# Optimization experiments

Measured on AMD Instinct MI355X. Metric: run time of the kernel, lower is better.

## Reference

```python
import jax, jax.numpy as jnp
import numpy as np

N_NODES = 100_000
N_EDGES = 1_600_000
IN_C, HID_C, OUT_C = 128, 64, 32


def gcn_conv(x, W, b, src, dst, n_nodes):
    """PyG GCNConv with add_self_loops=True, symmetric normalization.
    out = D^{-1/2} (A + I) D^{-1/2} (x @ W) + b, with D = deg(A) + 1.
    Self-loop contribution added analytically to avoid materializing loop edges."""
    h = x @ W                                            # [N, F_out]
    deg = jnp.zeros((n_nodes,), h.dtype).at[dst].add(1.0) + 1.0
    dinv = jax.lax.rsqrt(deg)                            # deg >= 1 from self-loops
    norm = dinv[src] * dinv[dst]                         # [E]
    agg = jnp.zeros_like(h).at[dst].add(h[src] * norm[:, None])
    agg = agg + h * (dinv * dinv)[:, None]               # self-loop term
    return agg + b


def setup_inputs() -> dict:
    key = jax.random.key(0)
    ks = jax.random.split(key, 9)
    x = jax.random.normal(ks[0], (N_NODES, IN_C), dtype=jnp.float32)
    edge_index = jax.random.randint(ks[1], (2, N_EDGES), 0, N_NODES, dtype=jnp.int64)
    g = lambda k, fi, fo: jax.random.normal(k, (fi, fo), jnp.float32) * np.sqrt(2.0 / (fi + fo)).astype(np.float32)
    W1 = g(ks[2], IN_C, HID_C)
    b1 = jnp.zeros((HID_C,), jnp.float32)
    W2 = g(ks[3], HID_C, OUT_C)
    b2 = jnp.zeros((OUT_C,), jnp.float32)
    Wl = g(ks[4], IN_C + HID_C + OUT_C, OUT_C)
    bl = jnp.zeros((OUT_C,), jnp.float32)
    return {"x": x, "edge_index": edge_index, "W1": W1, "b1": b1,
            "W2": W2, "b2": b2, "Wl": Wl, "bl": bl}


def reference(x, edge_index, W1, b1, W2, b2, Wl, bl):
    src, dst = edge_index[0], edge_index[1]
    n = x.shape[0]
    h1 = jax.nn.relu(gcn_conv(x, W1, b1, src, dst, n))   # dropout is identity in eval
    h2 = gcn_conv(h1, W2, b2, src, dst, n)
    cat = jnp.concatenate([x, h1, h2], axis=1)           # [N, in+hid+out]
    return jax.nn.log_softmax(cat @ Wl + bl, axis=-1)
```

## Files before the change

### kernel.cpp

```cpp
#include <hip/hip_runtime.h>
#include <hip/hip_bf16.h>
#include <hip/hip_fp16.h>

typedef __hip_bfloat16 bf16;
typedef __attribute__((ext_vector_type(8))) short short8;
typedef __attribute__((ext_vector_type(4))) float f32x4;

#define MFMA16(a, b, c) __builtin_amdgcn_mfma_f32_16x16x32_bf16((a), (b), (c), 0, 0, 0)

static __device__ __forceinline__ float ldf(const void* p, long long i, bool f32) {
    return f32 ? ((const float*)p)[i] : __bfloat162float(((const bf16*)p)[i]);
}

static __device__ __forceinline__ short f2bs(float v) {
    union { bf16 h; short s; } u; u.h = __float2bfloat16(v); return u.s;
}

static __device__ __forceinline__ unsigned int pack_bf16x2(float a, float b) {
    return (unsigned int)(unsigned short)f2bs(a) | ((unsigned int)(unsigned short)f2bs(b) << 16);
}

__global__ __launch_bounds__(256, 4)
void sniff_kernel(const void* __restrict__ x, const void* __restrict__ w,
                  const int* __restrict__ ei, int E, int* __restrict__ flags) {
    __shared__ int cnt;
    if (threadIdx.x == 0) cnt = 0;
    __syncthreads();
    if (blockIdx.x < 2) {
        const unsigned short* u = (const unsigned short*)(blockIdx.x == 0 ? x : w);
        int bad = 0;
        for (int i = threadIdx.x; i < 4096; i += 256) {
            unsigned e = (u[i] >> 7) & 0xFF;
            if (e >= 0xA0) bad++;
        }
        atomicAdd(&cnt, bad);
        __syncthreads();
        if (threadIdx.x == 0) flags[blockIdx.x] = (cnt > 16) ? 1 : 0;
    } else {
        int nz = 0;
        for (int i = threadIdx.x; i < 1024; i += 256)
            if (ei[2 * i + 1] != 0) nz++;
        atomicAdd(&cnt, nz);
        __syncthreads();
        if (threadIdx.x == 0) flags[2] = (cnt == 0) ? 1 : 0;
    }
}

static __device__ __forceinline__ int ld_src(const int* ei, int E, int e, bool i64) {
    return i64 ? ei[2 * e] : ei[e];
}
static __device__ __forceinline__ int ld_dst(const int* ei, int E, int e, bool i64) {
    return i64 ? ei[2 * (E + e)] : ei[E + e];
}


__global__ __launch_bounds__(256, 4)
void bhist_kernel(const int* __restrict__ ei, int E, const int* __restrict__ flags,
                  int shift, int NB, int* __restrict__ bucketCount) {
    __shared__ int h[256];
    for (int i = threadIdx.x; i < 256; i += 256) h[i] = 0;
    __syncthreads();
    bool i64 = flags[2] != 0;
    int base = blockIdx.x * 4096;
    for (int i = 0; i < 16; i++) {
        int e = base + i * 256 + threadIdx.x;
        if (e < E) atomicAdd(&h[ld_dst(ei, E, e, i64) >> shift], 1);
    }
    __syncthreads();
    for (int i = threadIdx.x; i < NB; i += 256)
        if (h[i]) atomicAdd(&bucketCount[i], h[i]);
}

__global__ __launch_bounds__(256, 4)
void bscan_kernel(const int* __restrict__ bucketCount, int NB,
                  int* __restrict__ bucketBase, int* __restrict__ bcursor, int E) {
    __shared__ int bs[256];
    int v = ((int)threadIdx.x < NB) ? bucketCount[threadIdx.x] : 0;
    bs[threadIdx.x] = v;
    __syncthreads();
    for (int off = 1; off < 256; off <<= 1) {
        int t = ((int)threadIdx.x >= off) ? bs[threadIdx.x - off] : 0;
        __syncthreads();
        bs[threadIdx.x] += t;
        __syncthreads();
    }
    int excl = bs[threadIdx.x] - v;
    if ((int)threadIdx.x < NB) { bucketBase[threadIdx.x] = excl; bcursor[threadIdx.x] = excl; }
    if (threadIdx.x == 0) bucketBase[NB] = E;
}

__global__ __launch_bounds__(256, 4)
void bpart_kernel(const int* __restrict__ ei, int E, const int* __restrict__ flags,
                  int shift, int NB, int* __restrict__ bcursor, int2* __restrict__ ebuf) {
    __shared__ int h[256];
    __shared__ int gofs[256];
    for (int i = threadIdx.x; i < 256; i += 256) h[i] = 0;
    __syncthreads();
    bool i64 = flags[2] != 0;
    int base = blockIdx.x * 4096;
    for (int i = 0; i < 16; i++) {
        int e = base + i * 256 + threadIdx.x;
        if (e < E) atomicAdd(&h[ld_dst(ei, E, e, i64) >> shift], 1);
    }
    __syncthreads();
    if ((int)threadIdx.x < NB) {
        int c = h[threadIdx.x];
        gofs[threadIdx.x] = c ? atomicAdd(&bcursor[threadIdx.x], c) : 0;
    }
    __syncthreads();
    for (int i = threadIdx.x; i < 256; i += 256) h[i] = 0;
    __syncthreads();
    for (int i = 0; i < 16; i++) {
        int e = base + i * 256 + threadIdx.x;
        if (e < E) {
            int s = ld_src(ei, E, e, i64), d = ld_dst(ei, E, e, i64);
            int b = d >> shift;
            int p = atomicAdd(&h[b], 1);
            ebuf[gofs[b] + p] = make_int2(s, d);
        }
    }
}

__global__ __launch_bounds__(256, 2)
void bbuild_kernel(const int2* __restrict__ ebuf, const int* __restrict__ bucketBase,
                   int shift, int N, int E, int* __restrict__ rowptr,
                   float* __restrict__ dinv, int* __restrict__ csr_src) {
    __shared__ int cnt[1024];
    __shared__ int exc[1024];
    __shared__ int bs[256];
    int b = blockIdx.x;
    int nodeBase = b << shift;
    int width = 1 << shift;
    int nn = N - nodeBase; if (nn > width) nn = width;
    int beg = bucketBase[b], end = bucketBase[b + 1];
    for (int i = threadIdx.x; i < width; i += 256) cnt[i] = 0;
    __syncthreads();
    for (int e = beg + threadIdx.x; e < end; e += 256)
        atomicAdd(&cnt[ebuf[e].y - nodeBase], 1);
    __syncthreads();
    int per = width / 256;
    int s = 0;
    int base4 = threadIdx.x * per;
    for (int i = 0; i < per; i++) s += cnt[base4 + i];
    bs[threadIdx.x] = s;
    __syncthreads();
    for (int off = 1; off < 256; off <<= 1) {
        int t = ((int)threadIdx.x >= off) ? bs[threadIdx.x - off] : 0;
        __syncthreads();
        bs[threadIdx.x] += t;
        __syncthreads();
    }
    int run = bs[threadIdx.x] - s;
    for (int i = 0; i < per; i++) { exc[base4 + i] = run; run += cnt[base4 + i]; }
    __syncthreads();
    for (int i = threadIdx.x; i < nn; i += 256) {
        int node = nodeBase + i;
        rowptr[node] = beg + exc[i];
        dinv[node] = rsqrtf((float)cnt[i] + 1.0f);
    }
    __syncthreads();
    for (int i = threadIdx.x; i < width; i += 256) cnt[i] = 0;
    __syncthreads();
    for (int e = beg + threadIdx.x; e < end; e += 256) {
        int2 v = ebuf[e];
        int l = v.y - nodeBase;
        int p = atomicAdd(&cnt[l], 1);
        csr_src[beg + exc[l] + p] = v.x;
    }
    if (b == 0 && threadIdx.x == 0) rowptr[N] = E;
}

__global__ __launch_bounds__(256, 4)
void repack_kernel(const void* __restrict__ W1, const void* __restrict__ W2,
                   const void* __restrict__ Wl, const int* __restrict__ flags,
                   bf16* __restrict__ Bp1, bf16* __restrict__ Bp2, bf16* __restrict__ Bp3) {
    bool fw = flags[1] != 0;
    const void* W; bf16* Bp; int ntiles, nc, nfrag;
    if (blockIdx.x == 0)      { W = W1; Bp = Bp1; ntiles = 4; nc = 64; nfrag = 16; }
    else if (blockIdx.x == 1) { W = W2; Bp = Bp2; ntiles = 2; nc = 32; nfrag = 4;  }
    else                      { W = Wl; Bp = Bp3; ntiles = 2; nc = 32; nfrag = 14; }
    for (int s = threadIdx.x; s < nfrag * 64; s += 256) {
        int f = s >> 6, lane = s & 63;
        int kstep = f / ntiles, ntile = f % ntiles;
        int n = ntile * 16 + (lane & 15);
        int kbase = kstep * 32 + (lane >> 4) * 8;
#pragma unroll
        for (int j = 0; j < 8; j++)
            Bp[s * 8 + j] = __float2bfloat16(ldf(W, (long long)(kbase + j) * nc + n, fw));
    }
}

__global__ __launch_bounds__(256, 4)
void cvt_x_kernel(const void* __restrict__ x, const int* __restrict__ flags,
                  short* __restrict__ xb, long long total8) {
    long long i = (long long)blockIdx.x * 256 + threadIdx.x;
    if (i >= total8) return;
    bool fx = flags[0] != 0;
    short8 o;
    if (fx) {
        const float4* xf = (const float4*)x;
        float4 a = xf[i * 2], b = xf[i * 2 + 1];
        o[0] = f2bs(a.x); o[1] = f2bs(a.y); o[2] = f2bs(a.z); o[3] = f2bs(a.w);
        o[4] = f2bs(b.x); o[5] = f2bs(b.y); o[6] = f2bs(b.z); o[7] = f2bs(b.w);
    } else {
        o = ((const short8*)x)[i];
    }
    ((short8*)xb)[i] = o;
}

__global__ __launch_bounds__(256, 3)
void gemm1_mfma_kernel(const short* __restrict__ xb, const bf16* __restrict__ Bpack,
                       const float* __restrict__ dinv, __half* __restrict__ h1g, int N) {
    int lane = threadIdx.x & 63, wave = threadIdx.x >> 6;
    int m = lane & 15, quad = lane >> 4;
    int base = blockIdx.x * 128 + wave * 32;
    if (base >= N) return;
    const short8* bp = (const short8*)Bpack;
    short8 B[16];
#pragma unroll
    for (int i = 0; i < 16; i++) B[i] = bp[i * 64 + lane];
    if (base + 32 <= N) {
#pragma unroll
        for (int t = 0; t < 2; t++) {
            int r0 = base + t * 16;
            const short* xr = &xb[(long long)(r0 + m) * 128 + quad * 8];
            short8 A[4];
#pragma unroll
            for (int k = 0; k < 4; k++) A[k] = *(const short8*)(xr + k * 32);
            f32x4 acc[4];
#pragma unroll
            for (int nt = 0; nt < 4; nt++) acc[nt] = (f32x4){0.f, 0.f, 0.f, 0.f};
#pragma unroll
            for (int k = 0; k < 4; k++) {
#pragma unroll
                for (int nt = 0; nt < 4; nt++) acc[nt] = MFMA16(A[k], B[k * 4 + nt], acc[nt]);
            }
            float dv[4];
#pragma unroll
            for (int r = 0; r < 4; r++) dv[r] = dinv[r0 + quad * 4 + r];
            __half* o = &h1g[(long long)(r0 + quad * 4) * 64 + m];
#pragma unroll
            for (int nt = 0; nt < 4; nt++) {
#pragma unroll
                for (int r = 0; r < 4; r++) o[(long long)r * 64 + nt * 16] = __float2half(acc[nt][r] * dv[r]);
            }
        }
    } else {
#pragma unroll
        for (int t = 0; t < 2; t++) {
            int r0 = base + t * 16;
            int row = r0 + m;
            short8 A[4];
#pragma unroll
            for (int k = 0; k < 4; k++) A[k] = (short8){0,0,0,0,0,0,0,0};
            if (row < N) {
                const short* xr = &xb[(long long)row * 128 + quad * 8];
#pragma unroll
                for (int k = 0; k < 4; k++) A[k] = *(const short8*)(xr + k * 32);
            }
            f32x4 acc[4];
#pragma unroll
            for (int nt = 0; nt < 4; nt++) acc[nt] = (f32x4){0.f, 0.f, 0.f, 0.f};
#pragma unroll
            for (int k = 0; k < 4; k++) {
#pragma unroll
                for (int nt = 0; nt < 4; nt++) acc[nt] = MFMA16(A[k], B[k * 4 + nt], acc[nt]);
            }
#pragma unroll
            for (int r = 0; r < 4; r++) {
                int orow = r0 + quad * 4 + r;
                if (orow < N) {
                    float dv = dinv[orow];
                    __half* o = &h1g[(long long)orow * 64 + m];
#pragma unroll
                    for (int nt = 0; nt < 4; nt++) o[nt * 16] = __float2half(acc[nt][r] * dv);
                }
            }
        }
    }
}

__global__ __launch_bounds__(256, 8)
void gather1_kernel(const unsigned int* __restrict__ h1g, const float* __restrict__ dinv,
                    const int* __restrict__ rowptr, const int* __restrict__ csr_src,
                    const void* __restrict__ b1, const int* __restrict__ flags,
                    unsigned int* __restrict__ h1b, int N) {
    bool fw = flags[1] != 0;
    int lane = threadIdx.x & 63;
    int c = lane & 31, hf = lane >> 5;
    int wv = __builtin_amdgcn_readfirstlane(threadIdx.x >> 6);
    int node = blockIdx.x * 4 + wv;
    if (node >= N) return;
    int beg = rowptr[node], end = rowptr[node + 1];
    float dvd = dinv[node];
    const unsigned int* hL = h1g + c;
    float a0 = 0.f, a1 = 0.f;
    for (int b = beg; b < end; b += 16) {
        unsigned int v[8]; float m[8];
#pragma unroll
        for (int u = 0; u < 8; u++) {
            int i0 = b + 2 * u, i1 = i0 + 1;
            int s0 = csr_src[(i0 < end) ? i0 : beg];
            int s1 = csr_src[(i1 < end) ? i1 : beg];
            float m0 = (i0 < end) ? 1.f : 0.f;
            float m1 = (i1 < end) ? 1.f : 0.f;
            int s = hf ? s1 : s0;
            m[u] = hf ? m1 : m0;
            v[u] = hL[(long long)s * 32];
        }
#pragma unroll
        for (int u = 0; u < 8; u++) {
            float2 f = __half22float2(*(const __half2*)&v[u]);
            a0 = fmaf(f.x, m[u], a0);
            a1 = fmaf(f.y, m[u], a1);
        }
    }
    a0 += __shfl_xor(a0, 32);
    a1 += __shfl_xor(a1, 32);
    if (hf == 0) {
        unsigned int gsv = h1g[(long long)node * 32 + c];
        float2 gs = __half22float2(*(const __half2*)&gsv);
        float o0 = dvd * (a0 + gs.x) + ldf(b1, 2 * c, fw);
        float o1 = dvd * (a1 + gs.y) + ldf(b1, 2 * c + 1, fw);
        h1b[(long long)node * 32 + c] = pack_bf16x2(fmaxf(o0, 0.f), fmaxf(o1, 0.f));
    }
}

__global__ __launch_bounds__(256, 4)
void gemm2_mfma_kernel(const short* __restrict__ h1b, const bf16* __restrict__ Bpack,
                       const float* __restrict__ dinv, __half* __restrict__ h2g, int N) {
    int lane = threadIdx.x & 63, wave = threadIdx.x >> 6;
    int m = lane & 15, quad = lane >> 4;
    int r0 = blockIdx.x * 64 + wave * 16;
    if (r0 >= N) return;
    const short8* bp = (const short8*)Bpack;
    short8 B[4];
#pragma unroll
    for (int i = 0; i < 4; i++) B[i] = bp[i * 64 + lane];
    f32x4 acc0 = {0.f,0.f,0.f,0.f}, acc1 = {0.f,0.f,0.f,0.f};
    if (r0 + 16 <= N) {
        const short* xr = &h1b[(long long)(r0 + m) * 64 + quad * 8];
#pragma unroll
        for (int k = 0; k < 2; k++) {
            short8 A = *(const short8*)(xr + k * 32);
            acc0 = MFMA16(A, B[k * 2 + 0], acc0);
            acc1 = MFMA16(A, B[k * 2 + 1], acc1);
        }
        float dv[4];
#pragma unroll
        for (int r = 0; r < 4; r++) dv[r] = dinv[r0 + quad * 4 + r];
        __half* o = &h2g[(long long)(r0 + quad * 4) * 32 + m];
#pragma unroll
        for (int r = 0; r < 4; r++) {
            o[(long long)r * 32]      = __float2half(acc0[r] * dv[r]);
            o[(long long)r * 32 + 16] = __float2half(acc1[r] * dv[r]);
        }
    } else {
        int row = r0 + m;
#pragma unroll
        for (int k = 0; k < 2; k++) {
            short8 A = {0,0,0,0,0,0,0,0};
            if (row < N) A = *(const short8*)&h1b[(long long)row * 64 + k * 32 + quad * 8];
            acc0 = MFMA16(A, B[k * 2 + 0], acc0);
            acc1 = MFMA16(A, B[k * 2 + 1], acc1);
        }
#pragma unroll
        for (int r = 0; r < 4; r++) {
            int orow = r0 + quad * 4 + r;
            if (orow < N) {
                float dv = dinv[orow];
                h2g[(long long)orow * 32 + m]      = __float2half(acc0[r] * dv);
                h2g[(long long)orow * 32 + 16 + m] = __float2half(acc1[r] * dv);
            }
        }
    }
}

__global__ __launch_bounds__(256, 8)
void gather2_kernel(const unsigned int* __restrict__ h2g, const float* __restrict__ dinv,
                    const int* __restrict__ rowptr, const int* __restrict__ csr_src,
                    const void* __restrict__ b2, const int* __restrict__ flags,
                    unsigned int* __restrict__ h2b, int N) {
    bool fw = flags[1] != 0;
    int lane = threadIdx.x & 63;
    int c = lane & 15, sub = lane >> 4;
    int wv = __builtin_amdgcn_readfirstlane(threadIdx.x >> 6);
    int node = blockIdx.x * 4 + wv;
    if (node >= N) return;
    int beg = rowptr[node], end = rowptr[node + 1];
    float dvd = dinv[node];
    const unsigned int* hL = h2g + c;
    float a0 = 0.f, a1 = 0.f;
    for (int b = beg; b < end; b += 16) {
        unsigned int v[4]; float m[4];
#pragma unroll
        for (int u = 0; u < 4; u++) {
            int i0 = b + 4 * u;
            int s0 = csr_src[(i0     < end) ? i0     : beg];
            int s1 = csr_src[(i0 + 1 < end) ? i0 + 1 : beg];
            int s2 = csr_src[(i0 + 2 < end) ? i0 + 2 : beg];
            int s3 = csr_src[(i0 + 3 < end) ? i0 + 3 : beg];
            int sa = (sub & 1) ? s1 : s0;
            int sb = (sub & 1) ? s3 : s2;
            int s  = (sub & 2) ? sb : sa;
            float ma = (sub & 1) ? ((i0 + 1 < end) ? 1.f : 0.f) : ((i0 < end) ? 1.f : 0.f);
            float mb = (sub & 1) ? ((i0 + 3 < end) ? 1.f : 0.f) : ((i0 + 2 < end) ? 1.f : 0.f);
            m[u] = (sub & 2) ? mb : ma;
            v[u] = hL[(long long)s * 16];
        }
#pragma unroll
        for (int u = 0; u < 4; u++) {
            float2 f = __half22float2(*(const __half2*)&v[u]);
            a0 = fmaf(f.x, m[u], a0);
            a1 = fmaf(f.y, m[u], a1);
        }
    }
    a0 += __shfl_xor(a0, 16); a1 += __shfl_xor(a1, 16);
    a0 += __shfl_xor(a0, 32); a1 += __shfl_xor(a1, 32);
    if (sub == 0) {
        unsigned int gsv = h2g[(long long)node * 16 + c];
        float2 gs = __half22float2(*(const __half2*)&gsv);
        float o0 = dvd * (a0 + gs.x) + ldf(b2, 2 * c, fw);
        float o1 = dvd * (a1 + gs.y) + ldf(b2, 2 * c + 1, fw);
        h2b[(long long)node * 16 + c] = pack_bf16x2(o0, o1);
    }
}

__global__ __launch_bounds__(256, 2)
void final_mfma_kernel(const short* __restrict__ xb, const short* __restrict__ h1b,
                       const short* __restrict__ h2b, const bf16* __restrict__ Bpack,
                       const void* __restrict__ bl, const int* __restrict__ flags,
                       void* __restrict__ out, int N) {
    bool fw = flags[1] != 0, fx = flags[0] != 0;
    int lane = threadIdx.x & 63, wave = threadIdx.x >> 6;
    int m = lane & 15, quad = lane >> 4;
    int r0 = blockIdx.x * 64 + wave * 16;
    if (r0 >= N) return;
    const short8* bp = (const short8*)Bpack;
    short8 B[14];
#pragma unroll
    for (int i = 0; i < 14; i++) B[i] = bp[i * 64 + lane];
    f32x4 acc0 = {0.f,0.f,0.f,0.f}, acc1 = {0.f,0.f,0.f,0.f};
    bool full = (r0 + 16 <= N);
    int row = r0 + m;
    bool rowok = full || (row < N);
#pragma unroll
    for (int s = 0; s < 7; s++) {
        short8 A = {0,0,0,0,0,0,0,0};
        if (rowok) {
            const short* p;
            if (s < 4)      p = &xb [(long long)row * 128 + s * 32 + quad * 8];
            else if (s < 6) p = &h1b[(long long)row * 64 + (s - 4) * 32 + quad * 8];
            else            p = &h2b[(long long)row * 32 + quad * 8];
            A = *(const short8*)p;
        }
        acc0 = MFMA16(A, B[s * 2 + 0], acc0);
        acc1 = MFMA16(A, B[s * 2 + 1], acc1);
    }
    float bl0 = ldf(bl, m, fw), bl1 = ldf(bl, m + 16, fw);
#pragma unroll
    for (int r = 0; r < 4; r++) {
        float v0 = acc0[r] + bl0, v1 = acc1[r] + bl1;
        float mx = fmaxf(v0, v1);
#pragma unroll
        for (int o = 8; o > 0; o >>= 1) mx = fmaxf(mx, __shfl_xor(mx, o));
        float sm = __expf(v0 - mx) + __expf(v1 - mx);
#pragma unroll
        for (int o = 8; o > 0; o >>= 1) sm += __shfl_xor(sm, o);
        float lse = mx + __logf(sm);
        int orow = r0 + quad * 4 + r;
        if (orow < N) {
            if (fx) {
                ((float*)out)[(long long)orow * 32 + m]      = v0 - lse;
                ((float*)out)[(long long)orow * 32 + 16 + m] = v1 - lse;
            } else {
                ((bf16*)out)[(long long)orow * 32 + m]      = __float2bfloat16(v0 - lse);
                ((bf16*)out)[(long long)orow * 32 + 16 + m] = __float2bfloat16(v1 - lse);
            }
        }
    }
}

extern "C" void kernel_launch(void* const* d_in, const int* in_sizes, int n_in,
                              void* d_out, int out_size, void* d_ws, size_t ws_size,
                              hipStream_t stream) {
    const void* x  = d_in[0];
    const int*  ei = (const int*)d_in[1];
    const void* W1 = d_in[2];
    const void* b1 = d_in[3];
    const void* W2 = d_in[4];
    const void* b2 = d_in[5];
    const void* Wl = d_in[6];
    const void* bl = d_in[7];

    int N = in_sizes[0] / 128;
    int E = in_sizes[1] / 2;

    int shift = 9;
    while (((N + (1 << shift) - 1) >> shift) > 256 && shift < 10) shift++;
    int NB = (N + (1 << shift) - 1) >> shift;

    int* ip      = (int*)d_ws;
    int* flags   = ip;
    int* bucketCount = ip + 16;
    int* bucketBase  = bucketCount + 256;
    int* bcursor     = bucketBase + 272;
    float* dinv  = (float*)(bcursor + 256);
    int* rowptr  = (int*)(dinv + N);
    bf16* Bp1    = (bf16*)(rowptr + N + 16);
    bf16* Bp2    = (bf16*)((int*)Bp1 + 4096);
    bf16* Bp3    = (bf16*)((int*)Bp2 + 1024);
    int* csr_src = (int*)Bp3 + 3584;
    short* xb    = (short*)(csr_src + E);
    int*   Ai    = (int*)xb + (size_t)N * 64;
    int2*  ebuf  = (int2*)Ai;
    __half* h1g  = (__half*)Ai;
    __half* h2g  = (__half*)Ai;
    unsigned int* h2b = (unsigned int*)(Ai + (size_t)N * 48);
    unsigned int* h1b = (unsigned int*)(Ai + (size_t)N * 64);

    hipMemsetAsync(ip, 0, (16 + 256) * sizeof(int), stream);

    sniff_kernel<<<3, 256, 0, stream>>>(x, W1, ei, E, flags);

    int nchunk = (E + 4095) / 4096;
    bhist_kernel<<<nchunk, 256, 0, stream>>>(ei, E, flags, shift, NB, bucketCount);
    bscan_kernel<<<1, 256, 0, stream>>>(bucketCount, NB, bucketBase, bcursor, E);
    bpart_kernel<<<nchunk, 256, 0, stream>>>(ei, E, flags, shift, NB, bcursor, ebuf);
    bbuild_kernel<<<NB, 256, 0, stream>>>(ebuf, bucketBase, shift, N, E, rowptr, dinv, csr_src);

    repack_kernel<<<3, 256, 0, stream>>>(W1, W2, Wl, flags, Bp1, Bp2, Bp3);

    long long total8 = (long long)N * 16;
    cvt_x_kernel<<<(int)((total8 + 255) / 256), 256, 0, stream>>>(x, flags, xb, total8);

    gemm1_mfma_kernel<<<(N + 127) / 128, 256, 0, stream>>>(xb, Bp1, dinv, h1g, N);
    gather1_kernel<<<(N + 3) / 4, 256, 0, stream>>>((const unsigned int*)h1g, dinv, rowptr, csr_src,
                                                    b1, flags, h1b, N);
    gemm2_mfma_kernel<<<(N + 63) / 64, 256, 0, stream>>>((const short*)h1b, Bp2, dinv, h2g, N);
    gather2_kernel<<<(N + 3) / 4, 256, 0, stream>>>((const unsigned int*)h2g, dinv, rowptr, csr_src,
                                                    b2, flags, h2b, N);
    final_mfma_kernel<<<(N + 63) / 64, 256, 0, stream>>>(xb, (const short*)h1b, (const short*)h2b,
                                                         Bp3, bl, flags, d_out, N);
}
```

Before: 324.8 us.

## Process two nodes per wave in gather kernels and cache edges in LDS during partition

Each wave in the two gather kernels now handles two destination nodes and interleaves their neighbor loads, so more independent gathers are in flight per wave and fewer blocks are launched. The edge-partition kernel stages the (src,dst) pairs in shared memory on the first pass instead of reading edge_index from global memory a second time. The cost is higher register pressure in the gathers, loop trip count set by the larger of the two degrees, and 32KB of LDS per partition block, which may limit occupancy.

New measurement: 330.1 us. Within noise of the previous version (+1.6%).

```diff
diff --git a/kernel.cpp b/kernel.cpp
--- a/kernel.cpp
+++ b/kernel.cpp
@@ -94,13 +94,18 @@
                   int shift, int NB, int* __restrict__ bcursor, int2* __restrict__ ebuf) {
     __shared__ int h[256];
     __shared__ int gofs[256];
+    __shared__ int2 se[4096];
     for (int i = threadIdx.x; i < 256; i += 256) h[i] = 0;
     __syncthreads();
     bool i64 = flags[2] != 0;
     int base = blockIdx.x * 4096;
     for (int i = 0; i < 16; i++) {
         int e = base + i * 256 + threadIdx.x;
-        if (e < E) atomicAdd(&h[ld_dst(ei, E, e, i64) >> shift], 1);
+        if (e < E) {
+            int s = ld_src(ei, E, e, i64), d = ld_dst(ei, E, e, i64);
+            se[i * 256 + threadIdx.x] = make_int2(s, d);
+            atomicAdd(&h[d >> shift], 1);
+        }
     }
     __syncthreads();
     if ((int)threadIdx.x < NB) {
@@ -113,10 +118,10 @@
     for (int i = 0; i < 16; i++) {
         int e = base + i * 256 + threadIdx.x;
         if (e < E) {
-            int s = ld_src(ei, E, e, i64), d = ld_dst(ei, E, e, i64);
-            int b = d >> shift;
+            int2 v = se[i * 256 + threadIdx.x];
+            int b = v.y >> shift;
             int p = atomicAdd(&h[b], 1);
-            ebuf[gofs[b] + p] = make_int2(s, d);
+            ebuf[gofs[b] + p] = v;
         }
     }
 }
@@ -283,45 +288,59 @@
 __global__ __launch_bounds__(256, 8)
 void gather1_kernel(const unsigned int* __restrict__ h1g, const float* __restrict__ dinv,
                     const int* __restrict__ rowptr, const int* __restrict__ csr_src,
-                    const void* __restrict__ b1, const int* __restrict__ flags,
+                    const void* __restrict__ bptr, const int* __restrict__ flags,
                     unsigned int* __restrict__ h1b, int N) {
     bool fw = flags[1] != 0;
     int lane = threadIdx.x & 63;
     int c = lane & 31, hf = lane >> 5;
     int wv = __builtin_amdgcn_readfirstlane(threadIdx.x >> 6);
-    int node = blockIdx.x * 4 + wv;
-    if (node >= N) return;
-    int beg = rowptr[node], end = rowptr[node + 1];
-    float dvd = dinv[node];
+    int n0 = blockIdx.x * 8 + wv * 2;
+    if (n0 >= N) return;
+    int n1 = (n0 + 1 < N) ? n0 + 1 : n0;
+    int beg0 = rowptr[n0], end0 = rowptr[n0 + 1];
+    int beg1 = rowptr[n1], end1 = rowptr[n1 + 1];
     const unsigned int* hL = h1g + c;
-    float a0 = 0.f, a1 = 0.f;
-    for (int b = beg; b < end; b += 16) {
-        unsigned int v[8]; float m[8];
+    float a00 = 0.f, a01 = 0.f, a10 = 0.f, a11 = 0.f;
+    int p0 = beg0, p1 = beg1;
+    while (p0 < end0 || p1 < end1) {
+        unsigned int v0[8], v1[8]; float m0[8], m1[8];
 #pragma unroll
         for (int u = 0; u < 8; u++) {
-            int i0 = b + 2 * u, i1 = i0 + 1;
-            int s0 = csr_src[(i0 < end) ? i0 : beg];
-            int s1 = csr_src[(i1 < end) ? i1 : beg];
-            float m0 = (i0 < end) ? 1.f : 0.f;
-            float m1 = (i1 < end) ? 1.f : 0.f;
-            int s = hf ? s1 : s0;
-            m[u] = hf ? m1 : m0;
-            v[u] = hL[(long long)s * 32];
+            int i00 = p0 + 2 * u, i01 = i00 + 1;
+            int s00 = csr_src[(i00 < end0) ? i00 : beg0];
+            int s01 = csr_src[(i01 < end0) ? i01 : beg0];
+            int sA = hf ? s01 : s00;
+            m0[u] = hf ? ((i01 < end0) ? 1.f : 0.f) : ((i00 < end0) ? 1.f : 0.f);
+            v0[u] = hL[(long long)sA * 32];
+            int i10 = p1 + 2 * u, i11 = i10 + 1;
+            int s10 = csr_src[(i10 < end1) ? i10 : beg1];
+            int s11 = csr_src[(i11 < end1) ? i11 : beg1];
+            int sB = hf ? s11 : s10;
+            m1[u] = hf ? ((i11 < end1) ? 1.f : 0.f) : ((i10 < end1) ? 1.f : 0.f);
+            v1[u] = hL[(long long)sB * 32];
         }
 #pragma unroll
         for (int u = 0; u < 8; u++) {
-            float2 f = __half22float2(*(const __half2*)&v[u]);
-            a0 = fmaf(f.x, m[u], a0);
-            a1 = fmaf(f.y, m[u], a1);
-        }
-    }
-    a0 += __shfl_xor(a0, 32);
-    a1 += __shfl_xor(a1, 32);
-    if (hf == 0) {
+            float2 f0 = __half22float2(*(const __half2*)&v0[u]);
+            a00 = fmaf(f0.x, m0[u], a00);
+            a01 = fmaf(f0.y, m0[u], a01);
+            float2 f1 = __half22float2(*(const __half2*)&v1[u]);
+            a10 = fmaf(f1.x, m1[u], a10);
+            a11 = fmaf(f1.y, m1[u], a11);
+        }
+        p0 += 16; p1 += 16;
+    }
+    a00 += __shfl_xor(a00, 32); a01 += __shfl_xor(a01, 32);
+    a10 += __shfl_xor(a10, 32); a11 += __shfl_xor(a11, 32);
+    int node = hf ? n1 : n0;
+    float a0 = hf ? a10 : a00;
+    float a1 = hf ? a11 : a01;
+    if (!(hf && n1 == n0)) {
         unsigned int gsv = h1g[(long long)node * 32 + c];
         float2 gs = __half22float2(*(const __half2*)&gsv);
-        float o0 = dvd * (a0 + gs.x) + ldf(b1, 2 * c, fw);
-        float o1 = dvd * (a1 + gs.y) + ldf(b1, 2 * c + 1, fw);
+        float dvd = dinv[node];
+        float o0 = dvd * (a0 + gs.x) + ldf(bptr, 2 * c, fw);
+        float o1 = dvd * (a1 + gs.y) + ldf(bptr, 2 * c + 1, fw);
         h1b[(long long)node * 32 + c] = pack_bf16x2(fmaxf(o0, 0.f), fmaxf(o1, 0.f));
     }
 }
@@ -379,49 +398,77 @@
 __global__ __launch_bounds__(256, 8)
 void gather2_kernel(const unsigned int* __restrict__ h2g, const float* __restrict__ dinv,
                     const int* __restrict__ rowptr, const int* __restrict__ csr_src,
-                    const void* __restrict__ b2, const int* __restrict__ flags,
+                    const void* __restrict__ bptr, const int* __restrict__ flags,
                     unsigned int* __restrict__ h2b, int N) {
     bool fw = flags[1] != 0;
     int lane = threadIdx.x & 63;
     int c = lane & 15, sub = lane >> 4;
     int wv = __builtin_amdgcn_readfirstlane(threadIdx.x >> 6);
-    int node = blockIdx.x * 4 + wv;
-    if (node >= N) return;
-    int beg = rowptr[node], end = rowptr[node + 1];
-    float dvd = dinv[node];
+    int n0 = blockIdx.x * 8 + wv * 2;
+    if (n0 >= N) return;
+    int n1 = (n0 + 1 < N) ? n0 + 1 : n0;
+    int beg0 = rowptr[n0], end0 = rowptr[n0 + 1];
+    int beg1 = rowptr[n1], end1 = rowptr[n1 + 1];
     const unsigned int* hL = h2g + c;
-    float a0 = 0.f, a1 = 0.f;
-    for (int b = beg; b < end; b += 16) {
-        unsigned int v[4]; float m[4];
+    float a00 = 0.f, a01 = 0.f, a10 = 0.f, a11 = 0.f;
+    int p0 = beg0, p1 = beg1;
+    while (p0 < end0 || p1 < end1) {
+        unsigned int v0[4], v1[4]; float m0[4], m1[4];
 #pragma unroll
         for (int u = 0; u < 4; u++) {
-            int i0 = b + 4 * u;
-            int s0 = csr_src[(i0     < end) ? i0     : beg];
-            int s1 = csr_src[(i0 + 1 < end) ? i0 + 1 : beg];
-            int s2 = csr_src[(i0 + 2 < end) ? i0 + 2 : beg];
-            int s3 = csr_src[(i0 + 3 < end) ? i0 + 3 : beg];
-            int sa = (sub & 1) ? s1 : s0;
-            int sb = (sub & 1) ? s3 : s2;
-            int s  = (sub & 2) ? sb : sa;
-            float ma = (sub & 1) ? ((i0 + 1 < end) ? 1.f : 0.f) : ((i0 < end) ? 1.f : 0.f);
-            float mb = (sub & 1) ? ((i0 + 3 < end) ? 1.f : 0.f) : ((i0 + 2 < end) ? 1.f : 0.f);
-            m[u] = (sub & 2) ? mb : ma;
-            v[u] = hL[(long long)s * 16];
+            {
+                int i0 = p0 + 4 * u;
+                int sa0 = csr_src[(i0     < end0) ? i0     : beg0];
+                int sa1 = csr_src[(i0 + 1 < end0) ? i0 + 1 : beg0];
+                int sa2 = csr_src[(i0 + 2 < end0) ? i0 + 2 : beg0];
+                int sa3 = csr_src[(i0 + 3 < end0) ? i0 + 3 : beg0];
+                int sA = (sub & 1) ? sa1 : sa0;
+                int sB = (sub & 1) ? sa3 : sa2;
+                int s  = (sub & 2) ? sB : sA;
+                float ma = (sub & 1) ? ((i0 + 1 < end0) ? 1.f : 0.f) : ((i0 < end0) ? 1.f : 0.f);
+                float mb = (sub & 1) ? ((i0 + 3 < end0) ? 1.f : 0.f) : ((i0 + 2 < end0) ? 1.f : 0.f);
+                m0[u] = (sub & 2) ? mb : ma;
+                v0[u] = hL[(long long)s * 16];
+            }
+            {
+                int i1 = p1 + 4 * u;
+                int sa0 = csr_src[(i1     < end1) ? i1     : beg1];
+                int sa1 = csr_src[(i1 + 1 < end1) ? i1 + 1 : beg1];
+                int sa2 = csr_src[(i1 + 2 < end1) ? i1 + 2 : beg1];
+                int sa3 = csr_src[(i1 + 3 < end1) ? i1 + 3 : beg1];
+                int sA = (sub & 1) ? sa1 : sa0;
+                int sB = (sub & 1) ? sa3 : sa2;
+                int s  = (sub & 2) ? sB : sA;
+                float ma = (sub & 1) ? ((i1 + 1 < end1) ? 1.f : 0.f) : ((i1 < end1) ? 1.f : 0.f);
+                float mb = (sub & 1) ? ((i1 + 3 < end1) ? 1.f : 0.f) : ((i1 + 2 < end1) ? 1.f : 0.f);
+                m1[u] = (sub & 2) ? mb : ma;
+                v1[u] = hL[(long long)s * 16];
+            }
         }
 #pragma unroll
         for (int u = 0; u < 4; u++) {
-            float2 f = __half22float2(*(const __half2*)&v[u]);
-            a0 = fmaf(f.x, m[u], a0);
-            a1 = fmaf(f.y, m[u], a1);
-        }
-    }
-    a0 += __shfl_xor(a0, 16); a1 += __shfl_xor(a1, 16);
-    a0 += __shfl_xor(a0, 32); a1 += __shfl_xor(a1, 32);
-    if (sub == 0) {
+            float2 f0 = __half22float2(*(const __half2*)&v0[u]);
+            a00 = fmaf(f0.x, m0[u], a00);
+            a01 = fmaf(f0.y, m0[u], a01);
+            float2 f1 = __half22float2(*(const __half2*)&v1[u]);
+            a10 = fmaf(f1.x, m1[u], a10);
+            a11 = fmaf(f1.y, m1[u], a11);
+        }
+        p0 += 16; p1 += 16;
+    }
+    a00 += __shfl_xor(a00, 16); a01 += __shfl_xor(a01, 16);
+    a10 += __shfl_xor(a10, 16); a11 += __shfl_xor(a11, 16);
+    a00 += __shfl_xor(a00, 32); a01 += __shfl_xor(a01, 32);
+    a10 += __shfl_xor(a10, 32); a11 += __shfl_xor(a11, 32);
+    if (sub < 2 && !(sub == 1 && n1 == n0)) {
+        int node = sub ? n1 : n0;
+        float a0 = sub ? a10 : a00;
+        float a1 = sub ? a11 : a01;
         unsigned int gsv = h2g[(long long)node * 16 + c];
         float2 gs = __half22float2(*(const __half2*)&gsv);
-        float o0 = dvd * (a0 + gs.x) + ldf(b2, 2 * c, fw);
-        float o1 = dvd * (a1 + gs.y) + ldf(b2, 2 * c + 1, fw);
+        float dvd = dinv[node];
+        float o0 = dvd * (a0 + gs.x) + ldf(bptr, 2 * c, fw);
+        float o1 = dvd * (a1 + gs.y) + ldf(bptr, 2 * c + 1, fw);
         h2b[(long long)node * 16 + c] = pack_bf16x2(o0, o1);
     }
 }
@@ -535,10 +582,10 @@
     cvt_x_kernel<<<(int)((total8 + 255) / 256), 256, 0, stream>>>(x, flags, xb, total8);
 
     gemm1_mfma_kernel<<<(N + 127) / 128, 256, 0, stream>>>(xb, Bp1, dinv, h1g, N);
-    gather1_kernel<<<(N + 3) / 4, 256, 0, stream>>>((const unsigned int*)h1g, dinv, rowptr, csr_src,
+    gather1_kernel<<<(N + 7) / 8, 256, 0, stream>>>((const unsigned int*)h1g, dinv, rowptr, csr_src,
                                                     b1, flags, h1b, N);
     gemm2_mfma_kernel<<<(N + 63) / 64, 256, 0, stream>>>((const short*)h1b, Bp2, dinv, h2g, N);
-    gather2_kernel<<<(N + 3) / 4, 256, 0, stream>>>((const unsigned int*)h2g, dinv, rowptr, csr_src,
+    gather2_kernel<<<(N + 7) / 8, 256, 0, stream>>>((const unsigned int*)h2g, dinv, rowptr, csr_src,
                                                     b2, flags, h2b, N);
     final_mfma_kernel<<<(N + 63) / 64, 256, 0, stream>>>(xb, (const short*)h1b, (const short*)h2b,
                                                          Bp3, bl, flags, d_out, N);
```
